# Kernel optimization log

Measured on AMD Instinct MI355X. Metric: run time of the kernel, lower is better.

The kernel has to match this reference:

```python
import jax, jax.numpy as jnp
import numpy as np

ROT_DIM = 32
THETA = 10000.0
HEAD_SIZE = 192


def _rope(t):
    # t: [B, T, D]; rotate first ROT_DIM features with interleaved-pair RoPE
    T = t.shape[1]
    inv_freq = 1.0 / (THETA ** (jnp.arange(0, ROT_DIM, 2, dtype=jnp.float32) / ROT_DIM))  # [16]
    freqs = jnp.arange(T, dtype=jnp.float32)[:, None] * inv_freq[None, :]  # [T,16]
    freqs = jnp.repeat(freqs, 2, axis=-1)  # [T,32], each freq repeated for the pair
    cos = jnp.cos(freqs).astype(t.dtype)
    sin = jnp.sin(freqs).astype(t.dtype)
    x = t[..., :ROT_DIM]
    x1 = x[..., 0::2]
    x2 = x[..., 1::2]
    rot_half = jnp.stack([-x2, x1], axis=-1).reshape(x.shape)  # interleave (-x2, x1)
    rotated = x * cos + rot_half * sin
    return jnp.concatenate([rotated, t[..., ROT_DIM:]], axis=-1)


def setup_inputs() -> dict:
    key = jax.random.key(0)
    k1, k2, k3, k4 = jax.random.split(key, 4)
    B, T, C, H = 64, 512, 768, HEAD_SIZE
    x = jax.random.normal(k1, (B, T, C), dtype=jnp.float32)
    s = 1.0 / np.sqrt(C)
    Wq = jax.random.normal(k2, (C, H), dtype=jnp.float32) * s
    Wk = jax.random.normal(k3, (C, H), dtype=jnp.float32) * s
    Wv = jax.random.normal(k4, (C, H), dtype=jnp.float32) * s
    return {"x": x, "Wq": Wq, "Wk": Wk, "Wv": Wv}


def reference(x, Wq, Wk, Wv):
    B, T, C = x.shape
    q = x @ Wq  # [B,T,H]
    k = x @ Wk
    v = x @ Wv
    q = _rope(q)
    k = _rope(k)
    scale = k.shape[-1] ** -0.5
    scores = jnp.einsum('bqh,bkh->bqk', q, k) * scale  # [B,T,T]
    causal = jnp.tril(jnp.ones((T, T), dtype=bool))
    scores = jnp.where(causal[None, :, :], scores, -jnp.inf)
    weight = jax.nn.softmax(scores, axis=-1)
    # dropout is identity at eval time
    out = jnp.einsum('bqk,bkh->bqh', weight, v)  # [B,T,H]
    return out
```

## Files before the change

kernel.cpp:

```cpp
#include <hip/hip_runtime.h>
#include <cstdint>

typedef __attribute__((ext_vector_type(8))) short short8;
typedef __attribute__((ext_vector_type(4))) float floatx4;

__device__ __forceinline__ unsigned short f2bf(float f) {
  uint32_t u = __builtin_bit_cast(uint32_t, f);
  u += 0x7fffu + ((u >> 16) & 1u);
  return (unsigned short)(u >> 16);
}

__global__ void prep_w_kernel(const float* __restrict__ Wq,
                              const float* __restrict__ Wk,
                              const float* __restrict__ Wv,
                              unsigned short* __restrict__ Wt) {
  int idx = blockIdx.x * 256 + threadIdx.x;
  if (idx >= 576 * 768) return;
  int n = idx / 768;
  int k = idx - n * 768;
  int which = n / 192;
  int nn = n - which * 192;
  const float* W = (which == 0) ? Wq : (which == 1) ? Wk : Wv;
  Wt[idx] = f2bf(W[k * 192 + nn]);
}

__global__ __launch_bounds__(256) void proj_kernel(
    const float* __restrict__ x, const unsigned short* __restrict__ Wt_all,
    unsigned short* __restrict__ q_ws, unsigned short* __restrict__ k_ws,
    unsigned short* __restrict__ v_ws) {
  __shared__ __align__(16) unsigned short A_lds[128 * 40];
  __shared__ __align__(16) unsigned short B_lds[192 * 40];
  const int tid = threadIdx.x;
  const int w = tid >> 6, l = tid & 63, quad = l >> 4, ln = l & 15;
  const int m0 = blockIdx.x * 128;
  const int which = blockIdx.y;
  const unsigned short* Wt = Wt_all + which * 192 * 768;

  floatx4 acc[2][12];
#pragma unroll
  for (int mt = 0; mt < 2; ++mt)
#pragma unroll
    for (int nt = 0; nt < 12; ++nt) acc[mt][nt] = floatx4{0.f, 0.f, 0.f, 0.f};

  for (int kb = 0; kb < 24; ++kb) {
    const int k0 = kb * 32;
#pragma unroll
    for (int it = 0; it < 4; ++it) {
      int qi = it * 256 + tid;
      int row = qi >> 3, c4 = qi & 7;
      float4 f = *(const float4*)(x + (size_t)(m0 + row) * 768 + k0 + c4 * 4);
      ushort4 p;
      p.x = f2bf(f.x); p.y = f2bf(f.y); p.z = f2bf(f.z); p.w = f2bf(f.w);
      *(ushort4*)&A_lds[row * 40 + c4 * 4] = p;
    }
#pragma unroll
    for (int it = 0; it < 3; ++it) {
      int idx = it * 256 + tid;
      int n = idx >> 2, c = idx & 3;
      uint4 v = *(const uint4*)(Wt + n * 768 + k0 + c * 8);
      *(uint4*)&B_lds[n * 40 + c * 8] = v;
    }
    __syncthreads();
    short8 a0 = *(const short8*)&A_lds[(w * 32 + ln) * 40 + quad * 8];
    short8 a1 = *(const short8*)&A_lds[(w * 32 + 16 + ln) * 40 + quad * 8];
#pragma unroll
    for (int nt = 0; nt < 12; ++nt) {
      short8 bfr = *(const short8*)&B_lds[(nt * 16 + ln) * 40 + quad * 8];
      acc[0][nt] = __builtin_amdgcn_mfma_f32_16x16x32_bf16(a0, bfr, acc[0][nt], 0, 0, 0);
      acc[1][nt] = __builtin_amdgcn_mfma_f32_16x16x32_bf16(a1, bfr, acc[1][nt], 0, 0, 0);
    }
    __syncthreads();
  }

#pragma unroll
  for (int mt = 0; mt < 2; ++mt) {
#pragma unroll
    for (int r = 0; r < 4; ++r) {
      int row_g = m0 + w * 32 + mt * 16 + quad * 4 + r;
      int t_pos = row_g & 511;
      float vals[12];
#pragma unroll
      for (int nt = 0; nt < 12; ++nt) vals[nt] = acc[mt][nt][r];
      if (which < 2) {
#pragma unroll
        for (int nt = 0; nt < 2; ++nt) {
          int col = nt * 16 + ln;
          float v = vals[nt];
          float pv = __shfl_xor(v, 1);
          int i = col >> 1;
          float inv_freq = exp2f(-(float)i * (13.287712379549449f / 16.0f));
          float ang = (float)t_pos * inv_freq;
          float sv, cv;
          sincosf(ang, &sv, &cv);
          vals[nt] = (col & 1) ? (v * cv + pv * sv) : (v * cv - pv * sv);
        }
      }
      if (which == 2) {
        int bb = row_g >> 9, t = row_g & 511;
#pragma unroll
        for (int nt = 0; nt < 12; ++nt)
          v_ws[(bb * 192 + nt * 16 + ln) * 512 + t] = f2bf(vals[nt]);
      } else {
        unsigned short* dst = (which == 0) ? q_ws : k_ws;
#pragma unroll
        for (int nt = 0; nt < 12; ++nt)
          dst[row_g * 192 + nt * 16 + ln] = f2bf(vals[nt]);
      }
    }
  }
}

__global__ __launch_bounds__(256) void attn_kernel(
    const unsigned short* __restrict__ q_ws, const unsigned short* __restrict__ k_ws,
    const unsigned short* __restrict__ v_ws, float* __restrict__ out) {
  __shared__ __align__(16) unsigned short K_lds[64 * 200];
  __shared__ __align__(16) unsigned short V_lds[192 * 72];
  __shared__ __align__(16) unsigned short P_lds[4][16 * 72];
  const int tid = threadIdx.x;
  const int w = tid >> 6, l = tid & 63, quad = l >> 4, ln = l & 15;
  const int qt = blockIdx.x, b = blockIdx.y;
  const int q0 = qt * 64;

  short8 qf[6];
  {
    const unsigned short* qp =
        q_ws + (size_t)(b * 512 + q0 + w * 16 + ln) * 192 + quad * 8;
#pragma unroll
    for (int kk = 0; kk < 6; ++kk) qf[kk] = *(const short8*)(qp + kk * 32);
  }

  float m_i[4], l_i[4];
  floatx4 o[12];
#pragma unroll
  for (int r = 0; r < 4; ++r) { m_i[r] = -1e30f; l_i[r] = 0.f; }
#pragma unroll
  for (int nt = 0; nt < 12; ++nt) o[nt] = floatx4{0.f, 0.f, 0.f, 0.f};
  const float sm_scale = 0.07216878364870323f;

  for (int kt = 0; kt <= qt; ++kt) {
    const int k0 = kt * 64;
    __syncthreads();
#pragma unroll
    for (int it = 0; it < 6; ++it) {
      int idx = it * 256 + tid;
      int row = idx / 24, c = idx - row * 24;
      uint4 v = *(const uint4*)(k_ws + (size_t)(b * 512 + k0 + row) * 192 + c * 8);
      *(uint4*)&K_lds[row * 200 + c * 8] = v;
    }
#pragma unroll
    for (int it = 0; it < 6; ++it) {
      int idx = it * 256 + tid;
      int row = idx >> 3, c = idx & 7;
      uint4 v = *(const uint4*)(v_ws + (size_t)(b * 192 + row) * 512 + k0 + c * 8);
      *(uint4*)&V_lds[row * 72 + c * 8] = v;
    }
    __syncthreads();

    float s[4][4];
#pragma unroll
    for (int nt = 0; nt < 4; ++nt) {
      floatx4 sa = floatx4{0.f, 0.f, 0.f, 0.f};
#pragma unroll
      for (int kk = 0; kk < 6; ++kk) {
        short8 kf = *(const short8*)&K_lds[(nt * 16 + ln) * 200 + kk * 32 + quad * 8];
        sa = __builtin_amdgcn_mfma_f32_16x16x32_bf16(qf[kk], kf, sa, 0, 0, 0);
      }
#pragma unroll
      for (int r = 0; r < 4; ++r) s[nt][r] = sa[r] * sm_scale;
    }
    if (kt == qt) {
#pragma unroll
      for (int nt = 0; nt < 4; ++nt)
#pragma unroll
        for (int r = 0; r < 4; ++r)
          if (nt * 16 + ln > w * 16 + quad * 4 + r) s[nt][r] = -1e30f;
    }
    float alpha[4];
#pragma unroll
    for (int r = 0; r < 4; ++r) {
      float mx = fmaxf(fmaxf(s[0][r], s[1][r]), fmaxf(s[2][r], s[3][r]));
      mx = fmaxf(mx, __shfl_xor(mx, 1));
      mx = fmaxf(mx, __shfl_xor(mx, 2));
      mx = fmaxf(mx, __shfl_xor(mx, 4));
      mx = fmaxf(mx, __shfl_xor(mx, 8));
      float mnew = fmaxf(m_i[r], mx);
      alpha[r] = __expf(m_i[r] - mnew);
      float sum = 0.f;
#pragma unroll
      for (int nt = 0; nt < 4; ++nt) {
        s[nt][r] = __expf(s[nt][r] - mnew);
        sum += s[nt][r];
      }
      sum += __shfl_xor(sum, 1);
      sum += __shfl_xor(sum, 2);
      sum += __shfl_xor(sum, 4);
      sum += __shfl_xor(sum, 8);
      l_i[r] = l_i[r] * alpha[r] + sum;
      m_i[r] = mnew;
    }
#pragma unroll
    for (int nt = 0; nt < 12; ++nt)
#pragma unroll
      for (int r = 0; r < 4; ++r) o[nt][r] *= alpha[r];

#pragma unroll
    for (int nt = 0; nt < 4; ++nt)
#pragma unroll
      for (int r = 0; r < 4; ++r)
        P_lds[w][(quad * 4 + r) * 72 + nt * 16 + ln] = f2bf(s[nt][r]);
    __asm__ volatile("s_waitcnt lgkmcnt(0)" ::: "memory");

#pragma unroll
    for (int ks = 0; ks < 2; ++ks) {
      short8 pf = *(const short8*)&P_lds[w][ln * 72 + ks * 32 + quad * 8];
#pragma unroll
      for (int nt = 0; nt < 12; ++nt) {
        short8 vf = *(const short8*)&V_lds[(nt * 16 + ln) * 72 + ks * 32 + quad * 8];
        o[nt] = __builtin_amdgcn_mfma_f32_16x16x32_bf16(pf, vf, o[nt], 0, 0, 0);
      }
    }
  }

#pragma unroll
  for (int r = 0; r < 4; ++r) {
    float inv = 1.0f / l_i[r];
    size_t rowoff = (size_t)(b * 512 + q0 + w * 16 + quad * 4 + r) * 192;
#pragma unroll
    for (int nt = 0; nt < 12; ++nt)
      out[rowoff + nt * 16 + ln] = o[nt][r] * inv;
  }
}

extern "C" void kernel_launch(void* const* d_in, const int* in_sizes, int n_in,
                              void* d_out, int out_size, void* d_ws, size_t ws_size,
                              hipStream_t stream) {
  const float* x = (const float*)d_in[0];
  const float* Wq = (const float*)d_in[1];
  const float* Wk = (const float*)d_in[2];
  const float* Wv = (const float*)d_in[3];
  float* out = (float*)d_out;

  char* ws = (char*)d_ws;
  const size_t QKV_BYTES = (size_t)64 * 512 * 192 * 2;
  unsigned short* q_ws = (unsigned short*)(ws);
  unsigned short* k_ws = (unsigned short*)(ws + QKV_BYTES);
  unsigned short* v_ws = (unsigned short*)(ws + 2 * QKV_BYTES);
  unsigned short* Wt = (unsigned short*)(ws + 3 * QKV_BYTES);

  hipLaunchKernelGGL(prep_w_kernel, dim3(1728), dim3(256), 0, stream, Wq, Wk, Wv, Wt);
  hipLaunchKernelGGL(proj_kernel, dim3(256, 3), dim3(256), 0, stream, x, Wt, q_ws, k_ws, v_ws);
  hipLaunchKernelGGL(attn_kernel, dim3(8, 64), dim3(256), 0, stream, q_ws, k_ws, v_ws, out);
}
```

Baseline: 270.6 us.

## Double-buffer projection GEMM and prefetch K/V tiles into registers in attention

The projection kernel now double-buffers its LDS tiles and loads the next x/W slice into registers while MFMAs run on the current one. It also packs bf16 conversion with a perm instruction (round-half-up rather than round-to-nearest-even) and writes V transposed as 4-wide vector stores. The attention kernel prefetches the next K/V tile into registers before the compute phase and reverses the q-tile order for half the batches to balance causal work across blocks. These changes aim to hide global-load latency, at the cost of higher register pressure and slightly different bf16 rounding.

```diff
diff --git a/kernel.cpp b/kernel.cpp
--- a/kernel.cpp
+++ b/kernel.cpp
@@ -8,6 +8,11 @@
   uint32_t u = __builtin_bit_cast(uint32_t, f);
   u += 0x7fffu + ((u >> 16) & 1u);
   return (unsigned short)(u >> 16);
+}
+__device__ __forceinline__ uint32_t pkbf(float lo, float hi) {
+  uint32_t a = __builtin_bit_cast(uint32_t, lo) + 0x8000u;
+  uint32_t b = __builtin_bit_cast(uint32_t, hi) + 0x8000u;
+  return __builtin_amdgcn_perm(b, a, 0x07060302);
 }
 
 __global__ void prep_w_kernel(const float* __restrict__ Wq,
@@ -28,60 +33,97 @@
     const float* __restrict__ x, const unsigned short* __restrict__ Wt_all,
     unsigned short* __restrict__ q_ws, unsigned short* __restrict__ k_ws,
     unsigned short* __restrict__ v_ws) {
-  __shared__ __align__(16) unsigned short A_lds[128 * 40];
-  __shared__ __align__(16) unsigned short B_lds[192 * 40];
+  __shared__ __align__(16) unsigned short A_lds[2][128 * 40];
+  __shared__ __align__(16) unsigned short B_lds[2][192 * 40];
   const int tid = threadIdx.x;
   const int w = tid >> 6, l = tid & 63, quad = l >> 4, ln = l & 15;
   const int m0 = blockIdx.x * 128;
   const int which = blockIdx.y;
   const unsigned short* Wt = Wt_all + which * 192 * 768;
 
+  const int arow = tid >> 3, ac4 = tid & 7;
+  const int brow = tid >> 2, bc = tid & 3;
+
   floatx4 acc[2][12];
 #pragma unroll
   for (int mt = 0; mt < 2; ++mt)
 #pragma unroll
     for (int nt = 0; nt < 12; ++nt) acc[mt][nt] = floatx4{0.f, 0.f, 0.f, 0.f};
 
+  float4 fa[4];
+  uint4 fb[3];
+#pragma unroll
+  for (int it = 0; it < 4; ++it)
+    fa[it] = *(const float4*)(x + (size_t)(m0 + arow + it * 32) * 768 + ac4 * 4);
+#pragma unroll
+  for (int it = 0; it < 3; ++it)
+    fb[it] = *(const uint4*)(Wt + (brow + it * 64) * 768 + bc * 8);
+#pragma unroll
+  for (int it = 0; it < 4; ++it) {
+    uint2 p = {pkbf(fa[it].x, fa[it].y), pkbf(fa[it].z, fa[it].w)};
+    *(uint2*)&A_lds[0][(arow + it * 32) * 40 + ac4 * 4] = p;
+  }
+#pragma unroll
+  for (int it = 0; it < 3; ++it)
+    *(uint4*)&B_lds[0][(brow + it * 64) * 40 + bc * 8] = fb[it];
+
   for (int kb = 0; kb < 24; ++kb) {
-    const int k0 = kb * 32;
-#pragma unroll
-    for (int it = 0; it < 4; ++it) {
-      int qi = it * 256 + tid;
-      int row = qi >> 3, c4 = qi & 7;
-      float4 f = *(const float4*)(x + (size_t)(m0 + row) * 768 + k0 + c4 * 4);
-      ushort4 p;
-      p.x = f2bf(f.x); p.y = f2bf(f.y); p.z = f2bf(f.z); p.w = f2bf(f.w);
-      *(ushort4*)&A_lds[row * 40 + c4 * 4] = p;
-    }
-#pragma unroll
-    for (int it = 0; it < 3; ++it) {
-      int idx = it * 256 + tid;
-      int n = idx >> 2, c = idx & 3;
-      uint4 v = *(const uint4*)(Wt + n * 768 + k0 + c * 8);
-      *(uint4*)&B_lds[n * 40 + c * 8] = v;
+    const int cur = kb & 1;
+    if (kb < 23) {
+      const int k1 = (kb + 1) * 32;
+#pragma unroll
+      for (int it = 0; it < 4; ++it)
+        fa[it] = *(const float4*)(x + (size_t)(m0 + arow + it * 32) * 768 + k1 + ac4 * 4);
+#pragma unroll
+      for (int it = 0; it < 3; ++it)
+        fb[it] = *(const uint4*)(Wt + (brow + it * 64) * 768 + k1 + bc * 8);
     }
     __syncthreads();
-    short8 a0 = *(const short8*)&A_lds[(w * 32 + ln) * 40 + quad * 8];
-    short8 a1 = *(const short8*)&A_lds[(w * 32 + 16 + ln) * 40 + quad * 8];
+    short8 a0 = *(const short8*)&A_lds[cur][(w * 32 + ln) * 40 + quad * 8];
+    short8 a1 = *(const short8*)&A_lds[cur][(w * 32 + 16 + ln) * 40 + quad * 8];
 #pragma unroll
     for (int nt = 0; nt < 12; ++nt) {
-      short8 bfr = *(const short8*)&B_lds[(nt * 16 + ln) * 40 + quad * 8];
+      short8 bfr = *(const short8*)&B_lds[cur][(nt * 16 + ln) * 40 + quad * 8];
       acc[0][nt] = __builtin_amdgcn_mfma_f32_16x16x32_bf16(a0, bfr, acc[0][nt], 0, 0, 0);
       acc[1][nt] = __builtin_amdgcn_mfma_f32_16x16x32_bf16(a1, bfr, acc[1][nt], 0, 0, 0);
     }
-    __syncthreads();
-  }
-
-#pragma unroll
-  for (int mt = 0; mt < 2; ++mt) {
-#pragma unroll
-    for (int r = 0; r < 4; ++r) {
-      int row_g = m0 + w * 32 + mt * 16 + quad * 4 + r;
-      int t_pos = row_g & 511;
-      float vals[12];
-#pragma unroll
-      for (int nt = 0; nt < 12; ++nt) vals[nt] = acc[mt][nt][r];
-      if (which < 2) {
+    if (kb < 23) {
+      const int nxt = cur ^ 1;
+#pragma unroll
+      for (int it = 0; it < 4; ++it) {
+        uint2 p = {pkbf(fa[it].x, fa[it].y), pkbf(fa[it].z, fa[it].w)};
+        *(uint2*)&A_lds[nxt][(arow + it * 32) * 40 + ac4 * 4] = p;
+      }
+#pragma unroll
+      for (int it = 0; it < 3; ++it)
+        *(uint4*)&B_lds[nxt][(brow + it * 64) * 40 + bc * 8] = fb[it];
+    }
+  }
+
+  if (which == 2) {
+#pragma unroll
+    for (int mt = 0; mt < 2; ++mt) {
+      int rb = m0 + w * 32 + mt * 16 + quad * 4;
+      int bb = rb >> 9, t = rb & 511;
+#pragma unroll
+      for (int nt = 0; nt < 12; ++nt) {
+        ushort4 pv;
+        pv.x = f2bf(acc[mt][nt][0]); pv.y = f2bf(acc[mt][nt][1]);
+        pv.z = f2bf(acc[mt][nt][2]); pv.w = f2bf(acc[mt][nt][3]);
+        *(ushort4*)&v_ws[((size_t)bb * 192 + nt * 16 + ln) * 512 + t] = pv;
+      }
+    }
+  } else {
+    unsigned short* dst = (which == 0) ? q_ws : k_ws;
+#pragma unroll
+    for (int mt = 0; mt < 2; ++mt) {
+#pragma unroll
+      for (int r = 0; r < 4; ++r) {
+        int row_g = m0 + w * 32 + mt * 16 + quad * 4 + r;
+        int t_pos = row_g & 511;
+        float vals[12];
+#pragma unroll
+        for (int nt = 0; nt < 12; ++nt) vals[nt] = acc[mt][nt][r];
 #pragma unroll
         for (int nt = 0; nt < 2; ++nt) {
           int col = nt * 16 + ln;
@@ -94,14 +136,6 @@
           sincosf(ang, &sv, &cv);
           vals[nt] = (col & 1) ? (v * cv + pv * sv) : (v * cv - pv * sv);
         }
-      }
-      if (which == 2) {
-        int bb = row_g >> 9, t = row_g & 511;
-#pragma unroll
-        for (int nt = 0; nt < 12; ++nt)
-          v_ws[(bb * 192 + nt * 16 + ln) * 512 + t] = f2bf(vals[nt]);
-      } else {
-        unsigned short* dst = (which == 0) ? q_ws : k_ws;
 #pragma unroll
         for (int nt = 0; nt < 12; ++nt)
           dst[row_g * 192 + nt * 16 + ln] = f2bf(vals[nt]);
@@ -118,8 +152,18 @@
   __shared__ __align__(16) unsigned short P_lds[4][16 * 72];
   const int tid = threadIdx.x;
   const int w = tid >> 6, l = tid & 63, quad = l >> 4, ln = l & 15;
-  const int qt = blockIdx.x, b = blockIdx.y;
+  const int b = blockIdx.y;
+  const int qt = (blockIdx.y < 32) ? blockIdx.x : 7 - blockIdx.x;
   const int q0 = qt * 64;
+
+  int krow[6], kcol[6];
+#pragma unroll
+  for (int it = 0; it < 6; ++it) {
+    int idx = it * 256 + tid;
+    krow[it] = idx / 24;
+    kcol[it] = idx - krow[it] * 24;
+  }
+  const int vrow = tid >> 3, vcol = tid & 7;
 
   short8 qf[6];
   {
@@ -137,22 +181,30 @@
   for (int nt = 0; nt < 12; ++nt) o[nt] = floatx4{0.f, 0.f, 0.f, 0.f};
   const float sm_scale = 0.07216878364870323f;
 
+  uint4 kreg[6], vreg[6];
+#pragma unroll
+  for (int it = 0; it < 6; ++it)
+    kreg[it] = *(const uint4*)(k_ws + (size_t)(b * 512 + krow[it]) * 192 + kcol[it] * 8);
+#pragma unroll
+  for (int it = 0; it < 6; ++it)
+    vreg[it] = *(const uint4*)(v_ws + (size_t)(b * 192 + vrow + it * 32) * 512 + vcol * 8);
+
   for (int kt = 0; kt <= qt; ++kt) {
-    const int k0 = kt * 64;
     __syncthreads();
 #pragma unroll
-    for (int it = 0; it < 6; ++it) {
-      int idx = it * 256 + tid;
-      int row = idx / 24, c = idx - row * 24;
-      uint4 v = *(const uint4*)(k_ws + (size_t)(b * 512 + k0 + row) * 192 + c * 8);
-      *(uint4*)&K_lds[row * 200 + c * 8] = v;
-    }
-#pragma unroll
-    for (int it = 0; it < 6; ++it) {
-      int idx = it * 256 + tid;
-      int row = idx >> 3, c = idx & 7;
-      uint4 v = *(const uint4*)(v_ws + (size_t)(b * 192 + row) * 512 + k0 + c * 8);
-      *(uint4*)&V_lds[row * 72 + c * 8] = v;
+    for (int it = 0; it < 6; ++it)
+      *(uint4*)&K_lds[krow[it] * 200 + kcol[it] * 8] = kreg[it];
+#pragma unroll
+    for (int it = 0; it < 6; ++it)
+      *(uint4*)&V_lds[(vrow + it * 32) * 72 + vcol * 8] = vreg[it];
+    if (kt < qt) {
+      const int k1 = (kt + 1) * 64;
+#pragma unroll
+      for (int it = 0; it < 6; ++it)
+        kreg[it] = *(const uint4*)(k_ws + (size_t)(b * 512 + k1 + krow[it]) * 192 + kcol[it] * 8);
+#pragma unroll
+      for (int it = 0; it < 6; ++it)
+        vreg[it] = *(const uint4*)(v_ws + (size_t)(b * 192 + vrow + it * 32) * 512 + k1 + vcol * 8);
     }
     __syncthreads();
 
```

Measured after the change: 316.6 us. 1.17x slower.
